# Optimization experiments

Hardware: AMD Instinct MI355X
Metric: run time of the kernel (lower is better)

## Reference

```python
import jax, jax.numpy as jnp
import numpy as np

MEM_SIZE = 131072
ENTRY_SIZE = 512
OUTPUT_SIZE = 512


def setup_inputs() -> dict:
    key = jax.random.key(0)
    ks = jax.random.split(key, 7)
    # NOTE: original initializes memory to zeros, which yields 0/0 NaNs in the
    # cosine distance; we use random memory state so the reference is finite.
    return {
        "x": jax.random.normal(ks[0], (1, ENTRY_SIZE), dtype=jnp.float32),
        "memory": jax.random.normal(ks[1], (MEM_SIZE, ENTRY_SIZE), dtype=jnp.float32),
        "w_key_gen": jax.random.normal(ks[2], (ENTRY_SIZE, ENTRY_SIZE), dtype=jnp.float32) * 0.05,
        "w_vect_gen": jax.random.normal(ks[3], (ENTRY_SIZE, ENTRY_SIZE), dtype=jnp.float32) * 0.05,
        "w_erase_gen": jax.random.normal(ks[4], (ENTRY_SIZE, ENTRY_SIZE), dtype=jnp.float32) * 0.05,
        "r_key_gen": jax.random.normal(ks[5], (ENTRY_SIZE, ENTRY_SIZE), dtype=jnp.float32) * 0.05,
        "post": jax.random.normal(ks[6], (2 * ENTRY_SIZE, OUTPUT_SIZE), dtype=jnp.float32) * 0.05,
    }


def _focus_by_content(memory, key):
    # Vectorized form of the per-slot cosine-similarity loop:
    # dist_m = <key, mem_m> / (||key|| * ||mem_m||), then normalize by the sum
    # (NOT a softmax -- faithful to the original).
    sims = (memory @ key) / (jnp.linalg.norm(key) * jnp.linalg.norm(memory, axis=1))  # (M,)
    return sims / jnp.sum(sims)


def reference(x, memory, w_key_gen, w_vect_gen, w_erase_gen, r_key_gen, post):
    x0 = x[0]  # (E,) -- original only uses the first row of the batch
    w_key = x0 @ w_key_gen      # (E,)
    r_key = x0 @ r_key_gen      # (E,)

    # Both addressing weights are computed on the PRE-write memory.
    w_weight = _focus_by_content(memory, w_key)  # (M,)
    r_weight = _focus_by_content(memory, r_key)  # (M,)

    erase = x0 @ w_erase_gen    # (E,)
    vect = x0 @ w_vect_gen      # (E,) computed but never written (bug kept faithfully)
    del vect

    # write_mem only erases: memory *= (1 - w_weight * erase)
    mem_new = memory * (1.0 - w_weight[:, None] * erase[None, :])  # (M, E)

    # read from post-write memory
    r_vect = jnp.sum(r_weight[:, None] * mem_new, axis=0)  # (E,)

    out = jnp.concatenate([x0, r_vect])[None, :] @ post  # (1, OUTPUT_SIZE)
    return out
```

## Files before the change

### kernel.cpp

```cpp
#include <hip/hip_runtime.h>

#define E 512
#define M_ROWS 131072
#define PROW 1026

__global__ __launch_bounds__(256) void k_keys(
    const float* __restrict__ x,
    const float* __restrict__ Wk,
    const float* __restrict__ Wr,
    const float* __restrict__ We,
    const float* __restrict__ post,
    float* __restrict__ keys)
{
    __shared__ float xs[E];
    __shared__ float red[256];
    const int t = threadIdx.x;
    for (int i = t; i < E; i += 256) xs[i] = x[i];
    __syncthreads();

    const int job = blockIdx.x >> 3;
    const float* Msel = (job == 0) ? Wk : (job == 1) ? Wr : (job == 2) ? We : post;
    const int cbase = (blockIdx.x & 7) << 6;
    const int c = cbase + (t & 63);
    const int r0 = (t >> 6) * 128;

    float s = 0.f;
    for (int i = r0; i < r0 + 128; ++i)
        s += xs[i] * Msel[(size_t)i * E + c];
    red[t] = s;
    __syncthreads();
    if (t < 64) {
        float v = red[t] + red[t + 64] + red[t + 128] + red[t + 192];
        keys[job * E + cbase + t] = v;
    }
}

__global__ __launch_bounds__(512) void k_main(
    const float* __restrict__ mem,
    const float* __restrict__ keys,
    float* __restrict__ partials)
{
    const int t    = threadIdx.x;
    const int lane = t & 63;
    const int wav  = t >> 6;
    const int gw   = blockIdx.x * 8 + wav;
    const int nw   = gridDim.x * 8;

    const int c0 = lane * 4;
    const int c1 = 256 + lane * 4;

    const float4 wk0 = *(const float4*)(keys + c0);
    const float4 wk1 = *(const float4*)(keys + c1);
    const float4 rk0 = *(const float4*)(keys + E + c0);
    const float4 rk1 = *(const float4*)(keys + E + c1);

    float4 a0 = {0.f,0.f,0.f,0.f}, a1 = {0.f,0.f,0.f,0.f};
    float4 b0 = {0.f,0.f,0.f,0.f}, b1 = {0.f,0.f,0.f,0.f};
    float sR = 0.f, sW = 0.f;

    for (int m = gw; m < M_ROWS; m += nw) {
        const float4 v0 = *(const float4*)(mem + (size_t)m * E + c0);
        const float4 v1 = *(const float4*)(mem + (size_t)m * E + c1);

        float dw = v0.x*wk0.x + v0.y*wk0.y + v0.z*wk0.z + v0.w*wk0.w
                 + v1.x*wk1.x + v1.y*wk1.y + v1.z*wk1.z + v1.w*wk1.w;
        float dr = v0.x*rk0.x + v0.y*rk0.y + v0.z*rk0.z + v0.w*rk0.w
                 + v1.x*rk1.x + v1.y*rk1.y + v1.z*rk1.z + v1.w*rk1.w;
        float n2 = v0.x*v0.x + v0.y*v0.y + v0.z*v0.z + v0.w*v0.w
                 + v1.x*v1.x + v1.y*v1.y + v1.z*v1.z + v1.w*v1.w;

        #pragma unroll
        for (int off = 32; off; off >>= 1) {
            dw += __shfl_xor(dw, off);
            dr += __shfl_xor(dr, off);
            n2 += __shfl_xor(n2, off);
        }
        const float inv  = rsqrtf(n2);
        const float simw = dw * inv;
        const float simr = dr * inv;
        sR += simr;
        sW += simw;
        const float u = simr * simw;

        a0.x += simr*v0.x; a0.y += simr*v0.y; a0.z += simr*v0.z; a0.w += simr*v0.w;
        a1.x += simr*v1.x; a1.y += simr*v1.y; a1.z += simr*v1.z; a1.w += simr*v1.w;
        b0.x += u*v0.x;    b0.y += u*v0.y;    b0.z += u*v0.z;    b0.w += u*v0.w;
        b1.x += u*v1.x;    b1.y += u*v1.y;    b1.z += u*v1.z;    b1.w += u*v1.w;
    }

    __shared__ float ldsA[E];
    __shared__ float ldsB[E];
    __shared__ float ldsS[2];
    for (int i = t; i < E; i += 512) { ldsA[i] = 0.f; ldsB[i] = 0.f; }
    if (t < 2) ldsS[t] = 0.f;
    __syncthreads();

    atomicAdd(&ldsA[c0+0], a0.x); atomicAdd(&ldsA[c0+1], a0.y);
    atomicAdd(&ldsA[c0+2], a0.z); atomicAdd(&ldsA[c0+3], a0.w);
    atomicAdd(&ldsA[c1+0], a1.x); atomicAdd(&ldsA[c1+1], a1.y);
    atomicAdd(&ldsA[c1+2], a1.z); atomicAdd(&ldsA[c1+3], a1.w);
    atomicAdd(&ldsB[c0+0], b0.x); atomicAdd(&ldsB[c0+1], b0.y);
    atomicAdd(&ldsB[c0+2], b0.z); atomicAdd(&ldsB[c0+3], b0.w);
    atomicAdd(&ldsB[c1+0], b1.x); atomicAdd(&ldsB[c1+1], b1.y);
    atomicAdd(&ldsB[c1+2], b1.z); atomicAdd(&ldsB[c1+3], b1.w);
    if (lane == 0) { atomicAdd(&ldsS[0], sR); atomicAdd(&ldsS[1], sW); }
    __syncthreads();

    float* p = partials + (size_t)blockIdx.x * PROW;
    for (int i = t; i < E; i += 512) { p[i] = ldsA[i]; p[E + i] = ldsB[i]; }
    if (t < 2) p[1024 + t] = ldsS[t];
}

__global__ __launch_bounds__(64) void k_reduce(
    const float* __restrict__ partials, float* __restrict__ R, int nb)
{
    const int c = blockIdx.x * 64 + threadIdx.x;
    if (c >= PROW) return;
    double s = 0.0;
    for (int b = 0; b < nb; ++b)
        s += (double)partials[(size_t)b * PROW + c];
    R[c] = (float)s;
}

__global__ __launch_bounds__(256) void k_out(
    const float* __restrict__ R,
    const float* __restrict__ keys,
    const float* __restrict__ post,
    float* __restrict__ out)
{
    __shared__ float rv[E];
    __shared__ float red[256];
    const int t = threadIdx.x;

    const float Sr = R[1024], Sw = R[1025];
    const float invSr   = 1.f / Sr;
    const float invSrSw = invSr / Sw;
    for (int e = t; e < E; e += 256)
        rv[e] = R[e] * invSr - keys[1024 + e] * R[E + e] * invSrSw;
    __syncthreads();

    const int j  = blockIdx.x * 64 + (t & 63);
    const int e0 = (t >> 6) * 128;
    float acc = 0.f;
    for (int e = e0; e < e0 + 128; ++e)
        acc += rv[e] * post[(size_t)(E + e) * E + j];
    red[t] = acc;
    __syncthreads();
    if (t < 64) {
        const int jj = blockIdx.x * 64 + t;
        out[jj] = red[t] + red[t + 64] + red[t + 128] + red[t + 192]
                + keys[1536 + jj];
    }
}

extern "C" void kernel_launch(void* const* d_in, const int* in_sizes, int n_in,
                              void* d_out, int out_size, void* d_ws, size_t ws_size,
                              hipStream_t stream)
{
    (void)in_sizes; (void)n_in; (void)out_size;
    const float* x    = (const float*)d_in[0];
    const float* mem  = (const float*)d_in[1];
    const float* Wk   = (const float*)d_in[2];
    const float* We   = (const float*)d_in[4];
    const float* Wr   = (const float*)d_in[5];
    const float* post = (const float*)d_in[6];
    float* out = (float*)d_out;
    float* ws  = (float*)d_ws;

    float* keys     = ws;
    float* partials = ws + 2048;

    long avail = (long)(ws_size / 4) - 2048 - PROW - 64;
    int nb = (int)(avail / PROW);
    if (nb > 512) nb = 512;
    if (nb < 1)  nb = 1;
    float* R = partials + (size_t)nb * PROW;

    hipLaunchKernelGGL(k_keys,   dim3(32), dim3(256), 0, stream,
                       x, Wk, Wr, We, post, keys);
    hipLaunchKernelGGL(k_main,   dim3(nb), dim3(512), 0, stream,
                       mem, keys, partials);
    hipLaunchKernelGGL(k_reduce, dim3((PROW + 63) / 64), dim3(64), 0, stream,
                       partials, R, nb);
    hipLaunchKernelGGL(k_out,    dim3(8), dim3(256), 0, stream,
                       R, keys, post, out);
}
```

Measured before the change: 615.9 us.

## Prefetch next memory row, double grid size, fuse partial reduction into output kernel

The main streaming loop now loads the next row's float4 values before computing on the current row. This software-pipelines the global loads to hide memory latency. The block cap rises from 512 to 1024, which gives more parallelism but produces more partials. The separate reduce kernel is removed: each of the 8 output blocks now sums all partials itself in double and then does the post matvec. That saves one launch, but the partial reduction is repeated redundantly across 8 blocks.

Result: slower. 770.8 us (+25.2%).

```diff
diff --git a/kernel.cpp b/kernel.cpp
--- a/kernel.cpp
+++ b/kernel.cpp
@@ -3,6 +3,7 @@
 #define E 512
 #define M_ROWS 131072
 #define PROW 1026
+#define NB_MAIN 1024
 
 __global__ __launch_bounds__(256) void k_keys(
     const float* __restrict__ x,
@@ -58,9 +59,22 @@
     float4 b0 = {0.f,0.f,0.f,0.f}, b1 = {0.f,0.f,0.f,0.f};
     float sR = 0.f, sW = 0.f;
 
-    for (int m = gw; m < M_ROWS; m += nw) {
-        const float4 v0 = *(const float4*)(mem + (size_t)m * E + c0);
-        const float4 v1 = *(const float4*)(mem + (size_t)m * E + c1);
+    const size_t step = (size_t)nw * E;
+    size_t base = (size_t)gw * E;
+
+    float4 v0 = {0.f,0.f,0.f,0.f}, v1 = {0.f,0.f,0.f,0.f};
+    if (gw < M_ROWS) {
+        v0 = *(const float4*)(mem + base + c0);
+        v1 = *(const float4*)(mem + base + c1);
+    }
+
+    for (int m = gw; m < M_ROWS; ) {
+        const int mn = m + nw;
+        float4 n0 = {0.f,0.f,0.f,0.f}, n1 = {0.f,0.f,0.f,0.f};
+        if (mn < M_ROWS) {
+            n0 = *(const float4*)(mem + base + step + c0);
+            n1 = *(const float4*)(mem + base + step + c1);
+        }
 
         float dw = v0.x*wk0.x + v0.y*wk0.y + v0.z*wk0.z + v0.w*wk0.w
                  + v1.x*wk1.x + v1.y*wk1.y + v1.z*wk1.z + v1.w*wk1.w;
@@ -86,6 +100,9 @@
         a1.x += simr*v1.x; a1.y += simr*v1.y; a1.z += simr*v1.z; a1.w += simr*v1.w;
         b0.x += u*v0.x;    b0.y += u*v0.y;    b0.z += u*v0.z;    b0.w += u*v0.w;
         b1.x += u*v1.x;    b1.y += u*v1.y;    b1.z += u*v1.z;    b1.w += u*v1.w;
+
+        v0 = n0; v1 = n1;
+        m = mn; base += step;
     }
 
     __shared__ float ldsA[E];
@@ -111,45 +128,47 @@
     if (t < 2) p[1024 + t] = ldsS[t];
 }
 
-__global__ __launch_bounds__(64) void k_reduce(
-    const float* __restrict__ partials, float* __restrict__ R, int nb)
-{
-    const int c = blockIdx.x * 64 + threadIdx.x;
-    if (c >= PROW) return;
-    double s = 0.0;
-    for (int b = 0; b < nb; ++b)
-        s += (double)partials[(size_t)b * PROW + c];
-    R[c] = (float)s;
-}
-
-__global__ __launch_bounds__(256) void k_out(
-    const float* __restrict__ R,
+__global__ __launch_bounds__(512) void k_out(
+    const float* __restrict__ partials,
     const float* __restrict__ keys,
     const float* __restrict__ post,
-    float* __restrict__ out)
+    float* __restrict__ out,
+    int nb)
 {
     __shared__ float rv[E];
-    __shared__ float red[256];
+    __shared__ float red[512];
+    __shared__ float SrSw[2];
     const int t = threadIdx.x;
 
-    const float Sr = R[1024], Sw = R[1025];
+    double sA = 0.0, sB = 0.0, sS = 0.0;
+    for (int b = 0; b < nb; ++b) {
+        const float* p = partials + (size_t)b * PROW;
+        sA += (double)p[t];
+        sB += (double)p[E + t];
+        if (t < 2) sS += (double)p[1024 + t];
+    }
+    if (t < 2) SrSw[t] = (float)sS;
+    __syncthreads();
+
+    const float Sr = SrSw[0], Sw = SrSw[1];
     const float invSr   = 1.f / Sr;
     const float invSrSw = invSr / Sw;
-    for (int e = t; e < E; e += 256)
-        rv[e] = R[e] * invSr - keys[1024 + e] * R[E + e] * invSrSw;
+    rv[t] = (float)sA * invSr - keys[1024 + t] * (float)sB * invSrSw;
     __syncthreads();
 
     const int j  = blockIdx.x * 64 + (t & 63);
-    const int e0 = (t >> 6) * 128;
+    const int e0 = (t >> 6) * 64;
     float acc = 0.f;
-    for (int e = e0; e < e0 + 128; ++e)
+    for (int e = e0; e < e0 + 64; ++e)
         acc += rv[e] * post[(size_t)(E + e) * E + j];
     red[t] = acc;
     __syncthreads();
     if (t < 64) {
+        float s = red[t];
+        #pragma unroll
+        for (int k = 1; k < 8; ++k) s += red[t + 64 * k];
         const int jj = blockIdx.x * 64 + t;
-        out[jj] = red[t] + red[t + 64] + red[t + 128] + red[t + 192]
-                + keys[1536 + jj];
+        out[jj] = s + keys[1536 + jj];
     }
 }
 
@@ -170,18 +189,15 @@
     float* keys     = ws;
     float* partials = ws + 2048;
 
-    long avail = (long)(ws_size / 4) - 2048 - PROW - 64;
+    long avail = (long)(ws_size / 4) - 2048 - 64;
     int nb = (int)(avail / PROW);
-    if (nb > 512) nb = 512;
+    if (nb > NB_MAIN) nb = NB_MAIN;
     if (nb < 1)  nb = 1;
-    float* R = partials + (size_t)nb * PROW;
-
-    hipLaunchKernelGGL(k_keys,   dim3(32), dim3(256), 0, stream,
+
+    hipLaunchKernelGGL(k_keys, dim3(32), dim3(256), 0, stream,
                        x, Wk, Wr, We, post, keys);
-    hipLaunchKernelGGL(k_main,   dim3(nb), dim3(512), 0, stream,
+    hipLaunchKernelGGL(k_main, dim3(nb), dim3(512), 0, stream,
                        mem, keys, partials);
-    hipLaunchKernelGGL(k_reduce, dim3((PROW + 63) / 64), dim3(64), 0, stream,
-                       partials, R, nb);
-    hipLaunchKernelGGL(k_out,    dim3(8), dim3(256), 0, stream,
-                       R, keys, post, out);
-}
+    hipLaunchKernelGGL(k_out,  dim3(8), dim3(512), 0, stream,
+                       partials, keys, post, out, nb);
+}
```
